# Kernel tuning notes

Measured on AMD Instinct MI355X. Metric: run time of the kernel, lower is better.

The kernel has to match this reference:

```python
import math
import jax, jax.numpy as jnp
import numpy as np

L, H, K, NH, V, DFF = 6, 512, 512, 8, 64, 1024
B, T, S = 8, 512, 512
PAD = 0


def _ln(x, g, b, eps=1e-5):
    m = jnp.mean(x, -1, keepdims=True)
    v = jnp.mean((x - m) ** 2, -1, keepdims=True)
    return (x - m) * jax.lax.rsqrt(v + eps) * g + b


def _mha(Q, Kin, Vin, mask, wq, bq, wk, bk, wv, bv, wo, bo, g, b):
    # weights stored [in, out]
    B_, Tq, Hd = Q.shape
    dk = wq.shape[1] // NH
    dv = wv.shape[1] // NH
    q = (Q @ wq + bq).reshape(B_, Tq, NH, dk).transpose(0, 2, 1, 3)
    k = (Kin @ wk + bk).reshape(B_, -1, NH, dk).transpose(0, 2, 1, 3)
    v = (Vin @ wv + bv).reshape(B_, -1, NH, dv).transpose(0, 2, 1, 3)
    scores = jnp.einsum('bhqd,bhkd->bhqk', q, k) / jnp.sqrt(jnp.float32(dk))
    scores = jnp.where(mask[:, None, :, :], jnp.float32(-1e9), scores)
    attn = jax.nn.softmax(scores, axis=-1)
    ctx = jnp.einsum('bhqk,bhkd->bhqd', attn, v).transpose(0, 2, 1, 3).reshape(B_, Tq, Hd)
    return _ln(ctx @ wo + bo + Q, g, b)


def _pe(t, d):
    pos = jnp.arange(t, dtype=jnp.float32)[:, None]
    div = jnp.exp(jnp.arange(0, d, 2, dtype=jnp.float32) * (-math.log(10000.0) / d))
    pe = jnp.zeros((t, d), jnp.float32)
    pe = pe.at[:, 0::2].set(jnp.sin(pos * div)).at[:, 1::2].set(jnp.cos(pos * div))
    return pe


def setup_inputs() -> dict:
    key = jax.random.key(0)
    ks = iter(jax.random.split(key, 40))
    nrm = lambda shape, s=0.02: jax.random.normal(next(ks), shape, jnp.float32) * s
    inp = {
        'smiles_index': jax.random.randint(next(ks), (B, T), 0, V, dtype=jnp.int32),
        'enc_outputs': jax.random.normal(next(ks), (B, S, H), jnp.float32),
        'enc_pad_mask': jnp.zeros((B, 1, S), bool),
        'tgt_len': T,
        'mol_emb': nrm((V, H), 1.0).at[PAD].set(0.0),  # padding_idx=0 row zeroed
        # self-attn stacks [L, ...]
        'sa_wq': nrm((L, H, K)), 'sa_bq': jnp.zeros((L, K)),
        'sa_wk': nrm((L, H, K)), 'sa_bk': jnp.zeros((L, K)),
        'sa_wv': nrm((L, H, H)), 'sa_bv': jnp.zeros((L, H)),
        'sa_wo': nrm((L, H, H)), 'sa_bo': jnp.zeros((L, H)),
        'ln1_g': jnp.ones((L, H)), 'ln1_b': jnp.zeros((L, H)),
        # cross-attn stacks
        'ea_wq': nrm((L, H, K)), 'ea_bq': jnp.zeros((L, K)),
        'ea_wk': nrm((L, H, K)), 'ea_bk': jnp.zeros((L, K)),
        'ea_wv': nrm((L, H, H)), 'ea_bv': jnp.zeros((L, H)),
        'ea_wo': nrm((L, H, H)), 'ea_bo': jnp.zeros((L, H)),
        'ln2_g': jnp.ones((L, H)), 'ln2_b': jnp.zeros((L, H)),
        # conv1x1 FFN == per-position linear
        'c1_w': nrm((L, H, DFF)), 'c1_b': jnp.zeros((L, DFF)),
        'c2_w': nrm((L, DFF, H)), 'c2_b': jnp.zeros((L, H)),
        'ln3_g': jnp.ones((L, H)), 'ln3_b': jnp.zeros((L, H)),
    }
    return inp


def reference(smiles_index, enc_outputs, enc_pad_mask, tgt_len, mol_emb,
              sa_wq, sa_bq, sa_wk, sa_bk, sa_wv, sa_bv, sa_wo, sa_bo, ln1_g, ln1_b,
              ea_wq, ea_bq, ea_wk, ea_bk, ea_wv, ea_bv, ea_wo, ea_bo, ln2_g, ln2_b,
              c1_w, c1_b, c2_w, c2_b, ln3_g, ln3_b):
    b, t = smiles_index.shape
    s = enc_outputs.shape[1]
    # embeddings + sinusoidal positional encoding (dropout is identity in eval)
    x = mol_emb[smiles_index] + _pe(t, mol_emb.shape[1])[None]
    # masks: pad (key == pad_id) OR causal upper-triangular
    pad = (smiles_index == PAD)[:, None, :]                 # [B,1,T] -> broadcast over queries
    causal = jnp.triu(jnp.ones((t, t), bool), 1)[None]      # [1,T,T]
    self_mask = pad | causal                                # [B,T,T]
    enc_mask = jnp.broadcast_to(enc_pad_mask, (b, t, s))    # [B,T,S]
    for l in range(L):
        x = _mha(x, x, x, self_mask,
                 sa_wq[l], sa_bq[l], sa_wk[l], sa_bk[l], sa_wv[l], sa_bv[l],
                 sa_wo[l], sa_bo[l], ln1_g[l], ln1_b[l])
        x = _mha(x, enc_outputs, enc_outputs, enc_mask,
                 ea_wq[l], ea_bq[l], ea_wk[l], ea_bk[l], ea_wv[l], ea_bv[l],
                 ea_wo[l], ea_bo[l], ln2_g[l], ln2_b[l])
        h = jax.nn.relu(x @ c1_w[l] + c1_b[l])
        y = h @ c2_w[l] + c2_b[l]
        x = _ln(y + x, ln3_g[l], ln3_b[l])
    return x
```

## Files before the change

### kernel.cpp

```cpp
#include <hip/hip_runtime.h>
#include <hip/hip_bf16.h>
#include <math.h>

#define NL   6
#define HD   512
#define NHD  8
#define DK   64
#define DFFN 1024
#define NB   8
#define TT   512
#define MROWS (NB*TT)
#define SQC  262144

typedef __hip_bfloat16 bf16;
typedef __attribute__((ext_vector_type(8))) short short8v;
typedef __attribute__((ext_vector_type(4))) short short4v;
typedef __attribute__((ext_vector_type(4))) float f32x4;

__device__ __forceinline__ float wave_sum(float v) {
#pragma unroll
  for (int off = 32; off; off >>= 1) v += __shfl_xor(v, off);
  return v;
}
__device__ __forceinline__ unsigned short f2bf(float x) {
  __hip_bfloat16 h = __float2bfloat16(x);
  return *reinterpret_cast<unsigned short*>(&h);
}
__device__ __forceinline__ float bf2f(unsigned short u) {
  return __uint_as_float(((unsigned)u) << 16);
}

struct Srcs8 { const float* s[8]; };
__global__ __launch_bounds__(256)
void wprep8_kernel(Srcs8 srcs, bf16* __restrict__ wt) {
  const int z = blockIdx.z;
  const int which = z & 7, l = z >> 3;
  const long long baseT[8] = {0, 0, 0, 18LL*SQC, 24LL*SQC, 30LL*SQC, 30LL*SQC, 42LL*SQC};
  const long long lstrT[8] = {3LL*SQC, 3LL*SQC, 3LL*SQC, SQC, SQC, 2LL*SQC, 2LL*SQC, SQC};
  const int rowOffT[8] = {0, 512, 1024, 0, 0, 0, 512, 0};

  __shared__ float t[32][33];
  const float* W = srcs.s[which] + (size_t)l * SQC;
  bf16* dst = wt + baseT[which] + (size_t)l * lstrT[which] + (size_t)rowOffT[which] * HD;
  const int n0 = blockIdx.x * 32, k0 = blockIdx.y * 32;
  const int tx = threadIdx.x & 31, ty = threadIdx.x >> 5;
#pragma unroll
  for (int j = 0; j < 4; ++j)
    t[ty + j * 8][tx] = W[(size_t)(k0 + ty + j * 8) * HD + n0 + tx];
  __syncthreads();
#pragma unroll
  for (int j = 0; j < 4; ++j)
    dst[(size_t)(n0 + ty + j * 8) * HD + k0 + tx] = __float2bfloat16(t[tx][ty + j * 8]);
}

__global__ __launch_bounds__(256)
void wprep_kernel(const float* __restrict__ W, bf16* __restrict__ Wt, int Kd, int Nd) {
  __shared__ float t[32][33];
  const size_t src = (size_t)blockIdx.z * Kd * Nd;
  const int n0 = blockIdx.x * 32, k0 = blockIdx.y * 32;
  const int tx = threadIdx.x & 31, ty = threadIdx.x >> 5;
#pragma unroll
  for (int j = 0; j < 4; ++j)
    t[ty + j * 8][tx] = W[src + (size_t)(k0 + ty + j * 8) * Nd + n0 + tx];
  __syncthreads();
#pragma unroll
  for (int j = 0; j < 4; ++j)
    Wt[src + (size_t)(n0 + ty + j * 8) * Kd + k0 + tx] = __float2bfloat16(t[tx][ty + j * 8]);
}

__global__ __launch_bounds__(256)
void bcat2_kernel(const float* __restrict__ b0, const float* __restrict__ b1,
                  const float* __restrict__ b2, const float* __restrict__ c0,
                  const float* __restrict__ c1, float* __restrict__ outS,
                  float* __restrict__ outKV) {
  const int l = blockIdx.x;
  if (blockIdx.y == 0) {
    for (int i = threadIdx.x; i < 1536; i += 256) {
      const int seg = i >> 9, off = i & 511;
      const float* src = seg == 0 ? b0 : (seg == 1 ? b1 : b2);
      outS[(size_t)l * 1536 + i] = src[(size_t)l * 512 + off];
    }
  } else {
    for (int i = threadIdx.x; i < 1024; i += 256) {
      const float* src = (i >> 9) == 0 ? c0 : c1;
      outKV[(size_t)l * 1024 + i] = src[(size_t)l * 512 + (i & 511)];
    }
  }
}

__global__ __launch_bounds__(256)
void cvtbf16_kernel(const float* __restrict__ in, unsigned short* __restrict__ out) {
  const int i = (blockIdx.x * 256 + threadIdx.x) * 4;
  float4 v = *(const float4*)(in + i);
  out[i + 0] = f2bf(v.x); out[i + 1] = f2bf(v.y);
  out[i + 2] = f2bf(v.z); out[i + 3] = f2bf(v.w);
}

__global__ __launch_bounds__(256)
void embed_pe_kernel(const int* __restrict__ idx, const float* __restrict__ emb,
                     float* __restrict__ x, unsigned short* __restrict__ xb) {
  const int row = blockIdx.x;
  const int t = row & (TT - 1);
  const int tok = idx[row];
  const float cdiv = -0.017988946009466842f;
#pragma unroll
  for (int e0 = 0; e0 < 2; ++e0) {
    const int e = threadIdx.x + e0 * 256;
    const float div = __expf((float)(e & ~1) * cdiv);
    const float ang = (float)t * div;
    const float pe = (e & 1) ? cosf(ang) : sinf(ang);
    const float v = emb[(size_t)tok * HD + e] + pe;
    x[(size_t)row * HD + e] = v;
    xb[(size_t)row * HD + e] = f2bf(v);
  }
}

__device__ __forceinline__ void gemm_compute(const char* As, const char* Bs,
                                             int wm, int wn, int lane,
                                             f32x4 (&acc)[2][2]) {
  const int rsw = (lane & 7) << 4;
  const int csel = (lane >> 4) * 16;
  short8v af[2][2], bfr[2][2];
#pragma unroll
  for (int m = 0; m < 2; ++m)
#pragma unroll
    for (int kk = 0; kk < 2; ++kk) {
      const int row = wm * 32 + m * 16 + (lane & 15);
      af[m][kk] = *(const short8v*)(As + row * 128 + ((kk * 64 + csel) ^ rsw));
    }
#pragma unroll
  for (int n = 0; n < 2; ++n)
#pragma unroll
    for (int kk = 0; kk < 2; ++kk) {
      const int row = wn * 32 + n * 16 + (lane & 15);
      bfr[n][kk] = *(const short8v*)(Bs + row * 128 + ((kk * 64 + csel) ^ rsw));
    }
#pragma unroll
  for (int m = 0; m < 2; ++m)
#pragma unroll
    for (int n = 0; n < 2; ++n) {
      acc[m][n] = __builtin_amdgcn_mfma_f32_16x16x32_bf16(af[m][0], bfr[n][0], acc[m][n], 0, 0, 0);
      acc[m][n] = __builtin_amdgcn_mfma_f32_16x16x32_bf16(af[m][1], bfr[n][1], acc[m][n], 0, 0, 0);
    }
}

template<int OUT_BF16, int RELU, int ADDRES>
__device__ __forceinline__
void mgemm_body(const bf16* __restrict__ A, const bf16* __restrict__ Bt,
                const float* __restrict__ bias, const float* __restrict__ res,
                float* __restrict__ Cf, unsigned short* __restrict__ Cb,
                int N, int K, int m0, int n0, char* As, char* Bs) {
  const int tid = threadIdx.x;
  const int w = tid >> 6, lane = tid & 63;
  const int wm = w >> 1, wn = w & 1;

  const int sr = w * 16 + (lane >> 3);
  const int scol = (lane & 7) * 16;
  const int swc = scol ^ ((sr & 7) << 4);
  const bf16* ga0 = A + (size_t)(m0 + sr) * K + (scol >> 1);
  const bf16* ga1 = A + (size_t)(m0 + sr + 8) * K + (scol >> 1);
  const bf16* gb0 = Bt + (size_t)(n0 + sr) * K + (scol >> 1);
  const bf16* gb1 = Bt + (size_t)(n0 + sr + 8) * K + (scol >> 1);
  char* la0 = As + sr * 128 + swc;
  char* la1 = As + (sr + 8) * 128 + swc;
  char* lb0 = Bs + sr * 128 + swc;
  char* lb1 = Bs + (sr + 8) * 128 + swc;

  f32x4 acc[2][2] = {};

  short8v ra0 = *(const short8v*)ga0, ra1 = *(const short8v*)ga1;
  short8v rb0 = *(const short8v*)gb0, rb1 = *(const short8v*)gb1;
  short8v sa0, sa1, sb0, sb1;

  for (int k0 = 0; k0 < K; k0 += 128) {
    __syncthreads();
    *(short8v*)la0 = ra0; *(short8v*)la1 = ra1;
    *(short8v*)lb0 = rb0; *(short8v*)lb1 = rb1;
    __syncthreads();
    sa0 = *(const short8v*)(ga0 + k0 + 64); sa1 = *(const short8v*)(ga1 + k0 + 64);
    sb0 = *(const short8v*)(gb0 + k0 + 64); sb1 = *(const short8v*)(gb1 + k0 + 64);
    gemm_compute(As, Bs, wm, wn, lane, acc);
    __syncthreads();
    *(short8v*)la0 = sa0; *(short8v*)la1 = sa1;
    *(short8v*)lb0 = sb0; *(short8v*)lb1 = sb1;
    __syncthreads();
    if (k0 + 128 < K) {
      ra0 = *(const short8v*)(ga0 + k0 + 128); ra1 = *(const short8v*)(ga1 + k0 + 128);
      rb0 = *(const short8v*)(gb0 + k0 + 128); rb1 = *(const short8v*)(gb1 + k0 + 128);
    }
    gemm_compute(As, Bs, wm, wn, lane, acc);
  }

  const int crow = (lane >> 4) * 4;
  const int ccol = lane & 15;
#pragma unroll
  for (int m = 0; m < 2; ++m)
#pragma unroll
    for (int n = 0; n < 2; ++n) {
      const int gr = m0 + wm * 32 + m * 16 + crow;
      const int gc = n0 + wn * 32 + n * 16 + ccol;
      const float bs = bias[gc];
#pragma unroll
      for (int r = 0; r < 4; ++r) {
        float v = acc[m][n][r] + bs;
        if (RELU) v = fmaxf(v, 0.f);
        if (ADDRES) v += res[(size_t)(gr + r) * N + gc];
        if (OUT_BF16) Cb[(size_t)(gr + r) * N + gc] = f2bf(v);
        else          Cf[(size_t)(gr + r) * N + gc] = v;
      }
    }
}

template<int OUT_BF16, int RELU, int ADDRES>
__global__ __launch_bounds__(256)
void mgemm_kernel(const bf16* __restrict__ A, const bf16* __restrict__ Bt,
                  const float* __restrict__ bias, const float* __restrict__ res,
                  float* __restrict__ Cf, unsigned short* __restrict__ Cb,
                  int N, int K) {
  __shared__ __attribute__((aligned(16))) char As[64 * 128];
  __shared__ __attribute__((aligned(16))) char Bs[64 * 128];
  mgemm_body<OUT_BF16, RELU, ADDRES>(A, Bt, bias, res, Cf, Cb, N, K,
                                     blockIdx.x * 64, blockIdx.y * 64, As, Bs);
}

__global__ __launch_bounds__(256)
void mgemm_eakv_kernel(const bf16* __restrict__ A, const bf16* __restrict__ BtBase,
                       const float* __restrict__ biasBase, unsigned short* __restrict__ CBase) {
  __shared__ __attribute__((aligned(16))) char As[128 * 128];
  __shared__ __attribute__((aligned(16))) char Bs[128 * 128];
  const int l = blockIdx.y >> 3, ny = blockIdx.y & 7;
  const bf16* Bt = BtBase + (size_t)l * 2 * SQC;
  const float* bias = biasBase + (size_t)l * 1024;
  unsigned short* C = CBase + (size_t)l * MROWS * 1024;
  const int m0 = blockIdx.x * 128, n0 = ny * 128;
  const int tid = threadIdx.x, w = tid >> 6, lane = tid & 63;
  const int wm = w >> 1, wn = w & 1;
  const int c8 = tid & 7, rg0 = tid >> 3;
  const int K = 512;

  const bf16* gA[4]; const bf16* gB[4];
  char* lA[4]; char* lB[4];
#pragma unroll
  for (int j = 0; j < 4; ++j) {
    const int r = rg0 + 32 * j;
    gA[j] = A  + (size_t)(m0 + r) * K + c8 * 8;
    gB[j] = Bt + (size_t)(n0 + r) * K + c8 * 8;
    const int swz = (c8 * 16) ^ ((r & 7) << 4);
    lA[j] = As + r * 128 + swz;
    lB[j] = Bs + r * 128 + swz;
  }

  f32x4 acc[4][4] = {};
  short8v rA[4], rB[4];
#pragma unroll
  for (int j = 0; j < 4; ++j) { rA[j] = *(const short8v*)gA[j]; rB[j] = *(const short8v*)gB[j]; }

  const int l4 = lane & 15, g = lane >> 4;
  for (int t = 0; t < 8; ++t) {
    __syncthreads();
#pragma unroll
    for (int j = 0; j < 4; ++j) { *(short8v*)lA[j] = rA[j]; *(short8v*)lB[j] = rB[j]; }
    __syncthreads();
    if (t + 1 < 8) {
#pragma unroll
      for (int j = 0; j < 4; ++j) {
        rA[j] = *(const short8v*)(gA[j] + (t + 1) * 64);
        rB[j] = *(const short8v*)(gB[j] + (t + 1) * 64);
      }
    }
#pragma unroll
    for (int kk = 0; kk < 2; ++kk) {
      short8v af[4], bv[4];
#pragma unroll
      for (int fm = 0; fm < 4; ++fm) {
        const int row = wm * 64 + fm * 16 + l4;
        af[fm] = *(const short8v*)(As + row * 128 + ((kk * 64 + g * 16) ^ ((row & 7) << 4)));
      }
#pragma unroll
      for (int fn = 0; fn < 4; ++fn) {
        const int row = wn * 64 + fn * 16 + l4;
        bv[fn] = *(const short8v*)(Bs + row * 128 + ((kk * 64 + g * 16) ^ ((row & 7) << 4)));
      }
#pragma unroll
      for (int fm = 0; fm < 4; ++fm)
#pragma unroll
        for (int fn = 0; fn < 4; ++fn)
          acc[fm][fn] = __builtin_amdgcn_mfma_f32_16x16x32_bf16(af[fm], bv[fn], acc[fm][fn], 0, 0, 0);
    }
  }

  const int crow = (lane >> 4) * 4, ccol = l4;
#pragma unroll
  for (int fm = 0; fm < 4; ++fm)
#pragma unroll
    for (int fn = 0; fn < 4; ++fn) {
      const int gr = m0 + wm * 64 + fm * 16 + crow;
      const int gc = n0 + wn * 64 + fn * 16 + ccol;
      const float bs = bias[gc];
#pragma unroll
      for (int r = 0; r < 4; ++r)
        C[(size_t)(gr + r) * 1024 + gc] = f2bf(acc[fm][fn][r] + bs);
    }
}

template<int CAUSAL>
__global__ __launch_bounds__(512)
void mattn_kernel(const unsigned short* __restrict__ q, const unsigned short* __restrict__ kgl,
                  const unsigned short* __restrict__ vgl, unsigned short* __restrict__ ctx,
                  const int* __restrict__ idx, const unsigned char* __restrict__ emask,
                  int qstride, int kvstride) {
  __shared__ __attribute__((aligned(16))) unsigned short kt[2][64 * 64];
  __shared__ __attribute__((aligned(16))) unsigned short vt[2][64 * 64];
  __shared__ __attribute__((aligned(16))) unsigned short pl[8][16 * 64];
  __shared__ float km[2][64];

  const int bh = blockIdx.x;
  const int b = bh >> 3, h = bh & 7;
  const int tid = threadIdx.x, w = tid >> 6, lane = tid & 63;
  const int l4 = lane & 15, g = lane >> 4;

  int qb_w;
  if (CAUSAL) {
    const int strip = (w < 4) ? blockIdx.y : 7 - blockIdx.y;
    qb_w = strip * 64 + (w & 3) * 16;
  } else {
    qb_w = blockIdx.y * 128 + w * 16;
  }
  const int kvEnd = CAUSAL ? (8 - blockIdx.y) * 64 : TT;

  const unsigned short* qp = q + (size_t)(b * TT + qb_w + l4) * qstride + h * DK + g * 8;
  short8v aq0 = *(const short8v*)qp;
  short8v aq1 = *(const short8v*)(qp + 32);

  const int sr_k = tid >> 3, sc8 = tid & 7;
  const unsigned short* kbp = kgl + (size_t)(b * TT + sr_k) * kvstride + h * DK + sc8 * 8;
  const int k2 = (tid & 31) * 2, d4 = (tid >> 5) * 4;
  const unsigned short* vbp0 = vgl + (size_t)(b * TT + k2) * kvstride + h * DK + d4;
  const unsigned short* vbp1 = vbp0 + kvstride;

  short8v rk = *(const short8v*)kbp;
  short4v rv0 = *(const short4v*)vbp0;
  short4v rv1 = *(const short4v*)vbp1;
  float mreg = 0.f;
  if (tid < 64) {
    const int kp = b * TT + tid;
    mreg = (CAUSAL ? (idx[kp] == 0) : (emask[kp] != 0)) ? -1e9f : 0.f;
  }

  float m_r[4], l_r[4];
  f32x4 acc_o[4];
#pragma unroll
  for (int r = 0; r < 4; ++r) { m_r[r] = -1e30f; l_r[r] = 0.f; }
#pragma unroll
  for (int f = 0; f < 4; ++f) acc_o[f] = (f32x4){0.f, 0.f, 0.f, 0.f};

  int tix = 0;
  for (int kt0 = 0; kt0 < kvEnd; kt0 += 64, ++tix) {
    const int buf = tix & 1;
    if (tid < 64) km[buf][tid] = mreg;
    *(short8v*)((char*)kt[buf] + sr_k * 128 + ((sc8 * 16) ^ ((sr_k & 7) << 4))) = rk;
#pragma unroll
    for (int j = 0; j < 4; ++j) {
      const int d = d4 + j;
      const unsigned pk = ((unsigned)(unsigned short)rv0[j]) | (((unsigned)(unsigned short)rv1[j]) << 16);
      *(unsigned*)((char*)vt[buf] + d * 128 + ((k2 * 2) ^ ((d & 7) << 4))) = pk;
    }
    __syncthreads();

    if (kt0 + 64 < kvEnd) {
      const size_t off = (size_t)(kt0 + 64) * kvstride;
      rk = *(const short8v*)(kbp + off);
      rv0 = *(const short4v*)(vbp0 + off);
      rv1 = *(const short4v*)(vbp1 + off);
      if (tid < 64) {
        const int kp = b * TT + kt0 + 64 + tid;
        mreg = (CAUSAL ? (idx[kp] == 0) : (emask[kp] != 0)) ? -1e9f : 0.f;
      }
    }

    if (!(CAUSAL && kt0 > qb_w + 15)) {
      const bool diag = CAUSAL && (kt0 + 64 > qb_w);

      f32x4 s4[4];
      __builtin_amdgcn_s_setprio(1);
#pragma unroll
      for (int f = 0; f < 4; ++f) {
        const int krow = f * 16 + l4;
        const int sw = (krow & 7) << 4;
        short8v bk0 = *(const short8v*)((const char*)kt[buf] + krow * 128 + ((g * 16) ^ sw));
        short8v bk1 = *(const short8v*)((const char*)kt[buf] + krow * 128 + ((64 + g * 16) ^ sw));
        f32x4 a = {};
        a = __builtin_amdgcn_mfma_f32_16x16x32_bf16(aq0, bk0, a, 0, 0, 0);
        a = __builtin_amdgcn_mfma_f32_16x16x32_bf16(aq1, bk1, a, 0, 0, 0);
        s4[f] = a;
      }
      __builtin_amdgcn_s_setprio(0);

      float kmb[4];
#pragma unroll
      for (int f = 0; f < 4; ++f) kmb[f] = km[buf][f * 16 + l4];

      float sc_r[4];
#pragma unroll
      for (int r = 0; r < 4; ++r) {
        const int qpos = qb_w + g * 4 + r;
        float sf[4];
#pragma unroll
        for (int f = 0; f < 4; ++f) sf[f] = fmaf(s4[f][r], 0.125f, kmb[f]);
        if (diag) {
#pragma unroll
          for (int f = 0; f < 4; ++f) {
            const int kpos = kt0 + f * 16 + l4;
            sf[f] = (kpos > qpos) ? -1e9f : sf[f];
          }
        }
        float mx = fmaxf(fmaxf(sf[0], sf[1]), fmaxf(sf[2], sf[3]));
#pragma unroll
        for (int off = 8; off; off >>= 1) mx = fmaxf(mx, __shfl_xor(mx, off));
        const float mn = fmaxf(m_r[r], mx);
        const float sc = __expf(m_r[r] - mn);
        m_r[r] = mn;
        sc_r[r] = sc;
        float ps = 0.f;
        const int prow = g * 4 + r;
        const int psw = (prow & 7) << 4;
#pragma unroll
        for (int f = 0; f < 4; ++f) {
          const float p = __expf(sf[f] - mn);
          ps += p;
          *(unsigned short*)((char*)pl[w] + prow * 128 + ((f * 32 + l4 * 2) ^ psw)) = f2bf(p);
        }
#pragma unroll
        for (int off = 8; off; off >>= 1) ps += __shfl_xor(ps, off);
        l_r[r] = l_r[r] * sc + ps;
      }

#pragma unroll
      for (int f = 0; f < 4; ++f)
#pragma unroll
        for (int r = 0; r < 4; ++r) acc_o[f][r] *= sc_r[r];

      const int asw = (l4 & 7) << 4;
      short8v pa0 = *(const short8v*)((const char*)pl[w] + l4 * 128 + ((g * 16) ^ asw));
      short8v pa1 = *(const short8v*)((const char*)pl[w] + l4 * 128 + ((g * 16 + 64) ^ asw));
      __builtin_amdgcn_s_setprio(1);
#pragma unroll
      for (int f = 0; f < 4; ++f) {
        const int drow = f * 16 + l4;
        const int sw = (drow & 7) << 4;
        short8v vb0 = *(const short8v*)((const char*)vt[buf] + drow * 128 + ((g * 16) ^ sw));
        short8v vb1 = *(const short8v*)((const char*)vt[buf] + drow * 128 + ((g * 16 + 64) ^ sw));
        acc_o[f] = __builtin_amdgcn_mfma_f32_16x16x32_bf16(pa0, vb0, acc_o[f], 0, 0, 0);
        acc_o[f] = __builtin_amdgcn_mfma_f32_16x16x32_bf16(pa1, vb1, acc_o[f], 0, 0, 0);
      }
      __builtin_amdgcn_s_setprio(0);
    }
  }

  float rl[4];
#pragma unroll
  for (int r = 0; r < 4; ++r) rl[r] = 1.f / l_r[r];
#pragma unroll
  for (int f = 0; f < 4; ++f)
#pragma unroll
    for (int r = 0; r < 4; ++r) {
      const int row = qb_w + g * 4 + r;
      const int col = h * DK + f * 16 + l4;
      ctx[(size_t)(b * TT + row) * HD + col] = f2bf(acc_o[f][r] * rl[r]);
    }
}

__global__ __launch_bounds__(256)
void ln2_kernel(const unsigned short* __restrict__ v, float* __restrict__ out,
                unsigned short* __restrict__ outb,
                const float* __restrict__ g, const float* __restrict__ bta) {
  const int row = blockIdx.x * 4 + (threadIdx.x >> 6);
  const int lane = threadIdx.x & 63;
  const size_t ro = (size_t)row * HD + lane * 8;

  short8v u = *(const short8v*)(v + ro);
  float f[8];
#pragma unroll
  for (int j = 0; j < 8; ++j) f[j] = bf2f((unsigned short)u[j]);

  float s = 0.f;
#pragma unroll
  for (int j = 0; j < 8; ++j) s += f[j];
  s = wave_sum(s);
  const float mean = s * (1.f / HD);

  float qv = 0.f;
#pragma unroll
  for (int j = 0; j < 8; ++j) { const float d = f[j] - mean; qv += d * d; }
  qv = wave_sum(qv);
  const float rstd = rsqrtf(qv * (1.f / HD) + 1e-5f);

  const float4 g0 = *(const float4*)(g + lane * 8);
  const float4 g1 = *(const float4*)(g + lane * 8 + 4);
  const float4 b0 = *(const float4*)(bta + lane * 8);
  const float4 b1 = *(const float4*)(bta + lane * 8 + 4);
  float gg[8] = {g0.x, g0.y, g0.z, g0.w, g1.x, g1.y, g1.z, g1.w};
  float bb[8] = {b0.x, b0.y, b0.z, b0.w, b1.x, b1.y, b1.z, b1.w};

  float o[8];
  short8v ob;
#pragma unroll
  for (int j = 0; j < 8; ++j) {
    o[j] = (f[j] - mean) * rstd * gg[j] + bb[j];
    ob[j] = (short)f2bf(o[j]);
  }
  *(float4*)(out + ro) = (float4){o[0], o[1], o[2], o[3]};
  *(float4*)(out + ro + 4) = (float4){o[4], o[5], o[6], o[7]};
  *(short8v*)(outb + ro) = ob;
}

extern "C" void kernel_launch(void* const* d_in, const int* in_sizes, int n_in,
                              void* d_out, int out_size, void* d_ws, size_t ws_size,
                              hipStream_t stream) {
  const int* idx = (const int*)d_in[0];
  const float* enc = (const float*)d_in[1];
  const unsigned char* emask = (const unsigned char*)d_in[2];
  const float* emb = (const float*)d_in[4];
  const float* sa_wq = (const float*)d_in[5];
  const float* sa_bq = (const float*)d_in[6];
  const float* sa_wk = (const float*)d_in[7];
  const float* sa_bk = (const float*)d_in[8];
  const float* sa_wv = (const float*)d_in[9];
  const float* sa_bv = (const float*)d_in[10];
  const float* sa_wo = (const float*)d_in[11];
  const float* sa_bo = (const float*)d_in[12];
  const float* ln1g = (const float*)d_in[13];
  const float* ln1b = (const float*)d_in[14];
  const float* ea_wq = (const float*)d_in[15];
  const float* ea_bq = (const float*)d_in[16];
  const float* ea_wk = (const float*)d_in[17];
  const float* ea_bk = (const float*)d_in[18];
  const float* ea_wv = (const float*)d_in[19];
  const float* ea_bv = (const float*)d_in[20];
  const float* ea_wo = (const float*)d_in[21];
  const float* ea_bo = (const float*)d_in[22];
  const float* ln2g = (const float*)d_in[23];
  const float* ln2b = (const float*)d_in[24];
  const float* c1w = (const float*)d_in[25];
  const float* c1b = (const float*)d_in[26];
  const float* c2w = (const float*)d_in[27];
  const float* c2b = (const float*)d_in[28];
  const float* ln3g = (const float*)d_in[29];
  const float* ln3b = (const float*)d_in[30];

  const size_t MH = (size_t)MROWS * HD;
  const size_t SQ = (size_t)SQC;
  char* ws = (char*)d_ws;
  float*          x    = (float*)(ws + 0);
  unsigned short* xb   = (unsigned short*)(ws + (8u << 20));
  unsigned short* qkvb = (unsigned short*)(ws + (12u << 20));
  unsigned short* qcb  = (unsigned short*)(ws + (24u << 20));
  unsigned short* cxb  = (unsigned short*)(ws + (28u << 20));
  unsigned short* ybb  = (unsigned short*)(ws + (32u << 20));
  unsigned short* encb = (unsigned short*)(ws + (36u << 20));
  bf16*           wt   = (bf16*)(ws + (40u << 20));
  float*          bcS  = (float*)(ws + (78u << 20));
  float*          bcKV = (float*)(ws + (79u << 20));
  unsigned short* kvb6 = (unsigned short*)(ws + (80u << 20));
  unsigned short* hb   = qkvb;

  bf16* t_saqkv = wt;
  bf16* t_sao   = wt + 18 * SQ;
  bf16* t_eaq   = wt + 24 * SQ;
  bf16* t_eakv  = wt + 30 * SQ;
  bf16* t_eao   = wt + 42 * SQ;
  bf16* t_c1    = wt + 48 * SQ;
  bf16* t_c2    = wt + 60 * SQ;

  const dim3 blk(256);
  const dim3 blk512(512);
  const dim3 gQKV(MROWS / 64, 1536 / 64);
  const dim3 g1024(MROWS / 64, 1024 / 64);
  const dim3 g512(MROWS / 64, 512 / 64);
  const dim3 gEAKV(MROWS / 128, 48);
  const dim3 gLN(MROWS / 4);
  const dim3 attng(NB * NHD, 4);

  Srcs8 s8;
  s8.s[0] = sa_wq; s8.s[1] = sa_wk; s8.s[2] = sa_wv; s8.s[3] = sa_wo;
  s8.s[4] = ea_wq; s8.s[5] = ea_wk; s8.s[6] = ea_wv; s8.s[7] = ea_wo;
  wprep8_kernel<<<dim3(16, 16, 48), blk, 0, stream>>>(s8, wt);
  wprep_kernel<<<dim3(32, 16, NL), blk, 0, stream>>>(c1w, t_c1, HD, DFFN);
  wprep_kernel<<<dim3(16, 32, NL), blk, 0, stream>>>(c2w, t_c2, DFFN, HD);
  bcat2_kernel<<<dim3(NL, 2), blk, 0, stream>>>(sa_bq, sa_bk, sa_bv, ea_bk, ea_bv, bcS, bcKV);
  cvtbf16_kernel<<<MH / 1024, blk, 0, stream>>>(enc, encb);
  mgemm_eakv_kernel<<<gEAKV, blk, 0, stream>>>((const bf16*)encb, t_eakv, bcKV, kvb6);

  embed_pe_kernel<<<MROWS, blk, 0, stream>>>(idx, emb, x, xb);

  for (int l = 0; l < NL; ++l) {
    const size_t b512 = (size_t)l * HD;
    const size_t bFF = (size_t)l * DFFN;
    float* lnout = (l == NL - 1) ? (float*)d_out : x;
    unsigned short* kvl = kvb6 + (size_t)l * MROWS * 1024;

    mgemm_kernel<1, 0, 0><<<gQKV, blk, 0, stream>>>(
        (const bf16*)xb, t_saqkv + (size_t)l * 3 * SQ, bcS + (size_t)l * 1536,
        nullptr, nullptr, qkvb, 1536, HD);
    mattn_kernel<1><<<attng, blk512, 0, stream>>>(qkvb, qkvb + 512, qkvb + 1024, cxb,
                                                  idx, emask, 1536, 1536);
    mgemm_kernel<1, 0, 1><<<g512, blk, 0, stream>>>(
        (const bf16*)cxb, t_sao + (size_t)l * SQ, sa_bo + b512, x, nullptr, ybb, HD, HD);
    ln2_kernel<<<gLN, blk, 0, stream>>>(ybb, x, xb, ln1g + b512, ln1b + b512);

    mgemm_kernel<1, 0, 0><<<g512, blk, 0, stream>>>(
        (const bf16*)xb, t_eaq + (size_t)l * SQ, ea_bq + b512, nullptr, nullptr, qcb, HD, HD);
    mattn_kernel<0><<<attng, blk512, 0, stream>>>(qcb, kvl, kvl + 512, cxb,
                                                  idx, emask, 512, 1024);
    mgemm_kernel<1, 0, 1><<<g512, blk, 0, stream>>>(
        (const bf16*)cxb, t_eao + (size_t)l * SQ, ea_bo + b512, x, nullptr, ybb, HD, HD);
    ln2_kernel<<<gLN, blk, 0, stream>>>(ybb, x, xb, ln2g + b512, ln2b + b512);

    mgemm_kernel<1, 1, 0><<<g1024, blk, 0, stream>>>(
        (const bf16*)xb, t_c1 + (size_t)l * 2 * SQ, c1b + bFF, nullptr, nullptr, hb, DFFN, HD);
    mgemm_kernel<1, 0, 1><<<g512, blk, 0, stream>>>(
        (const bf16*)hb, t_c2 + (size_t)l * 2 * SQ, c2b + b512, x, nullptr, ybb, HD, DFFN);
    ln2_kernel<<<gLN, blk, 0, stream>>>(ybb, lnout, xb, ln3g + b512, ln3b + b512);
  }
}
```

Measured before the change: 795.9 us.

## Fuse Q projection into attention kernels for self and cross attention

Each attention block now computes its own 128x64 Q tile from the bf16 activations and the per-head Q weight slice using MFMA through swizzled LDS, then adds the bias. This removes the separate cross-attention Q GEMM launch and shrinks the self-attention QKV GEMM to a KV-only GEMM. The Q intermediate no longer makes a round trip through global memory. In exchange it adds about 24 KB of LDS per block, which may lower occupancy, and a serial projection prologue before the attention loop. The attention grid has only 256 blocks, so the projection runs at limited parallelism.

```diff
diff --git a/kernel.cpp b/kernel.cpp
--- a/kernel.cpp
+++ b/kernel.cpp
@@ -305,32 +305,84 @@
 
 template<int CAUSAL>
 __global__ __launch_bounds__(512)
-void mattn_kernel(const unsigned short* __restrict__ q, const unsigned short* __restrict__ kgl,
-                  const unsigned short* __restrict__ vgl, unsigned short* __restrict__ ctx,
-                  const int* __restrict__ idx, const unsigned char* __restrict__ emask,
-                  int qstride, int kvstride) {
+void mattn_kernel(const unsigned short* __restrict__ xq, const bf16* __restrict__ qw,
+                  const float* __restrict__ qbias,
+                  const unsigned short* __restrict__ kgl, const unsigned short* __restrict__ vgl,
+                  unsigned short* __restrict__ ctx,
+                  const int* __restrict__ idx, const unsigned char* __restrict__ emask) {
   __shared__ __attribute__((aligned(16))) unsigned short kt[2][64 * 64];
   __shared__ __attribute__((aligned(16))) unsigned short vt[2][64 * 64];
   __shared__ __attribute__((aligned(16))) unsigned short pl[8][16 * 64];
+  __shared__ __attribute__((aligned(16))) unsigned short xs[128 * 64];
+  __shared__ __attribute__((aligned(16))) unsigned short ws2[64 * 64];
   __shared__ float km[2][64];
 
+  const int kvstride = 1024;
   const int bh = blockIdx.x;
   const int b = bh >> 3, h = bh & 7;
   const int tid = threadIdx.x, w = tid >> 6, lane = tid & 63;
   const int l4 = lane & 15, g = lane >> 4;
 
-  int qb_w;
+  int qb_w, xrow_base;
   if (CAUSAL) {
     const int strip = (w < 4) ? blockIdx.y : 7 - blockIdx.y;
     qb_w = strip * 64 + (w & 3) * 16;
+    xrow_base = (w >> 2) * 64 + (w & 3) * 16;
   } else {
     qb_w = blockIdx.y * 128 + w * 16;
+    xrow_base = w * 16;
   }
   const int kvEnd = CAUSAL ? (8 - blockIdx.y) * 64 : TT;
 
-  const unsigned short* qp = q + (size_t)(b * TT + qb_w + l4) * qstride + h * DK + g * 8;
-  short8v aq0 = *(const short8v*)qp;
-  short8v aq1 = *(const short8v*)(qp + 32);
+  f32x4 qacc[4] = {};
+  for (int t = 0; t < 8; ++t) {
+    __syncthreads();
+#pragma unroll
+    for (int cc = 0; cc < 2; ++cc) {
+      const int c = tid + cc * 512;
+      const int r = c >> 3, ch = c & 7;
+      int grow;
+      if (CAUSAL) grow = b * TT + ((r >> 6) ? (7 - blockIdx.y) : blockIdx.y) * 64 + (r & 63);
+      else        grow = b * TT + blockIdx.y * 128 + r;
+      short8v v = *(const short8v*)(xq + (size_t)grow * HD + t * 64 + ch * 8);
+      *(short8v*)((char*)xs + r * 128 + ((ch * 16) ^ ((r & 7) << 4))) = v;
+    }
+    {
+      const int r = tid >> 3, ch = tid & 7;
+      short8v v = *(const short8v*)(qw + (size_t)(h * 64 + r) * HD + t * 64 + ch * 8);
+      *(short8v*)((char*)ws2 + r * 128 + ((ch * 16) ^ ((r & 7) << 4))) = v;
+    }
+    __syncthreads();
+    __builtin_amdgcn_s_setprio(1);
+#pragma unroll
+    for (int kk = 0; kk < 2; ++kk) {
+      const int arow = xrow_base + l4;
+      short8v af = *(const short8v*)((char*)xs + arow * 128 + ((kk * 64 + g * 16) ^ ((arow & 7) << 4)));
+#pragma unroll
+      for (int fn = 0; fn < 4; ++fn) {
+        const int brow = fn * 16 + l4;
+        short8v bf = *(const short8v*)((char*)ws2 + brow * 128 + ((kk * 64 + g * 16) ^ ((brow & 7) << 4)));
+        qacc[fn] = __builtin_amdgcn_mfma_f32_16x16x32_bf16(af, bf, qacc[fn], 0, 0, 0);
+      }
+    }
+    __builtin_amdgcn_s_setprio(0);
+  }
+  __syncthreads();
+#pragma unroll
+  for (int fn = 0; fn < 4; ++fn) {
+    const int col = fn * 16 + l4;
+    const float bs = qbias[h * 64 + col];
+#pragma unroll
+    for (int r = 0; r < 4; ++r) {
+      const int row = xrow_base + (lane >> 4) * 4 + r;
+      *(unsigned short*)((char*)xs + row * 128 + ((col * 2) ^ ((row & 7) << 4))) = f2bf(qacc[fn][r] + bs);
+    }
+  }
+  __syncthreads();
+  const int arow2 = xrow_base + l4;
+  const int asw2 = (arow2 & 7) << 4;
+  short8v aq0 = *(const short8v*)((char*)xs + arow2 * 128 + ((g * 16) ^ asw2));
+  short8v aq1 = *(const short8v*)((char*)xs + arow2 * 128 + ((64 + g * 16) ^ asw2));
 
   const int sr_k = tid >> 3, sc8 = tid & 7;
   const unsigned short* kbp = kgl + (size_t)(b * TT + sr_k) * kvstride + h * DK + sc8 * 8;
@@ -554,7 +606,6 @@
   float*          x    = (float*)(ws + 0);
   unsigned short* xb   = (unsigned short*)(ws + (8u << 20));
   unsigned short* qkvb = (unsigned short*)(ws + (12u << 20));
-  unsigned short* qcb  = (unsigned short*)(ws + (24u << 20));
   unsigned short* cxb  = (unsigned short*)(ws + (28u << 20));
   unsigned short* ybb  = (unsigned short*)(ws + (32u << 20));
   unsigned short* encb = (unsigned short*)(ws + (36u << 20));
@@ -574,7 +625,7 @@
 
   const dim3 blk(256);
   const dim3 blk512(512);
-  const dim3 gQKV(MROWS / 64, 1536 / 64);
+  const dim3 gKV(MROWS / 64, 1024 / 64);
   const dim3 g1024(MROWS / 64, 1024 / 64);
   const dim3 g512(MROWS / 64, 512 / 64);
   const dim3 gEAKV(MROWS / 128, 48);
@@ -598,20 +649,19 @@
     const size_t bFF = (size_t)l * DFFN;
     float* lnout = (l == NL - 1) ? (float*)d_out : x;
     unsigned short* kvl = kvb6 + (size_t)l * MROWS * 1024;
-
-    mgemm_kernel<1, 0, 0><<<gQKV, blk, 0, stream>>>(
-        (const bf16*)xb, t_saqkv + (size_t)l * 3 * SQ, bcS + (size_t)l * 1536,
-        nullptr, nullptr, qkvb, 1536, HD);
-    mattn_kernel<1><<<attng, blk512, 0, stream>>>(qkvb, qkvb + 512, qkvb + 1024, cxb,
-                                                  idx, emask, 1536, 1536);
+    bf16* saslab = t_saqkv + (size_t)l * 3 * SQ;
+
+    mgemm_kernel<1, 0, 0><<<gKV, blk, 0, stream>>>(
+        (const bf16*)xb, saslab + (size_t)512 * HD, bcS + (size_t)l * 1536 + 512,
+        nullptr, nullptr, qkvb, 1024, HD);
+    mattn_kernel<1><<<attng, blk512, 0, stream>>>(xb, saslab, bcS + (size_t)l * 1536,
+                                                  qkvb, qkvb + 512, cxb, idx, emask);
     mgemm_kernel<1, 0, 1><<<g512, blk, 0, stream>>>(
         (const bf16*)cxb, t_sao + (size_t)l * SQ, sa_bo + b512, x, nullptr, ybb, HD, HD);
     ln2_kernel<<<gLN, blk, 0, stream>>>(ybb, x, xb, ln1g + b512, ln1b + b512);
 
-    mgemm_kernel<1, 0, 0><<<g512, blk, 0, stream>>>(
-        (const bf16*)xb, t_eaq + (size_t)l * SQ, ea_bq + b512, nullptr, nullptr, qcb, HD, HD);
-    mattn_kernel<0><<<attng, blk512, 0, stream>>>(qcb, kvl, kvl + 512, cxb,
-                                                  idx, emask, 512, 1024);
+    mattn_kernel<0><<<attng, blk512, 0, stream>>>(xb, t_eaq + (size_t)l * SQ, ea_bq + b512,
+                                                  kvl, kvl + 512, cxb, idx, emask);
     mgemm_kernel<1, 0, 1><<<g512, blk, 0, stream>>>(
         (const bf16*)cxb, t_eao + (size_t)l * SQ, ea_bo + b512, x, nullptr, ybb, HD, HD);
     ln2_kernel<<<gLN, blk, 0, stream>>>(ybb, x, xb, ln2g + b512, ln2b + b512);
```

Measured after the change: 811.8 us. 1.02x slower.
